# Performance work log

Measured on AMD Instinct MI355X. Metric: run time of the kernel, lower is better.

Reference implementation:

```python
import jax, jax.numpy as jnp
import numpy as np

T = 0.1  # temperature (init kwarg)
NEG_INF = -1e9


def setup_inputs() -> dict:
    key = jax.random.key(0)
    k1, k2 = jax.random.split(key)
    B, N, D = 4096, 2, 128
    feats = jax.random.normal(k1, (B, N, D), dtype=jnp.float32)
    labels = jax.random.randint(k2, (B,), 0, 512, dtype=jnp.int64)
    return {"feats": feats, "labels": labels}


def reference(feats, labels):
    B, N, D = feats.shape
    M = B * N
    f = feats.reshape(M, D)
    # F.normalize(dim=1): L2 normalize rows with eps clamp
    norm = jnp.maximum(jnp.linalg.norm(f, axis=1, keepdims=True), 1e-12)
    f = f / norm
    # labels.unsqueeze(1).repeat(1, N).view(-1)
    lab = jnp.repeat(labels, N)  # [M]
    mask = (lab[:, None] == lab[None, :]).astype(f.dtype)  # [M, M]
    logits = (f @ f.T) / T  # [M, M]
    logits_mask = 1.0 - jnp.eye(M, dtype=f.dtype)
    mask = mask * logits_mask  # drop self-pairs
    logits = logits * logits_mask + NEG_INF * (1.0 - logits_mask)
    log_prob = logits - jax.nn.logsumexp(logits, axis=1, keepdims=True)
    mean_pos = (mask * log_prob).sum(axis=1) / mask.sum(axis=1)
    return -mean_pos.mean()
```

## Files before the change

kernel.cpp:

```cpp
#include <hip/hip_runtime.h>
#include <math.h>

#define DD 128
#define NSPLIT 24
#define NBINS 512
#define SHIFT 10.0f
#define L2E_T 14.4269504089f

#define AS1 __attribute__((address_space(1)))
#define AS3 __attribute__((address_space(3)))

typedef _Float16 f16x8 __attribute__((ext_vector_type(8)));
typedef _Float16 f16x2 __attribute__((ext_vector_type(2)));
typedef float f32x4 __attribute__((ext_vector_type(4)));

__device__ __forceinline__ float ex2(float x) {
#if __has_builtin(__builtin_amdgcn_exp2f)
    return __builtin_amdgcn_exp2f(x);
#else
    return exp2f(x);
#endif
}

__global__ __launch_bounds__(256)
void zero_kernel(int* __restrict__ hist, float* __restrict__ out)
{
    hist[threadIdx.x] = 0;
    hist[256 + threadIdx.x] = 0;
    if (threadIdx.x == 0) out[0] = 0.f;
}

__global__ __launch_bounds__(256)
void norm_kernel(const float* __restrict__ f, const int* __restrict__ labels,
                 _Float16* __restrict__ fh, int* __restrict__ labm,
                 int* __restrict__ hist, int M, int nrep)
{
    int gw = (blockIdx.x * 256 + threadIdx.x) >> 6;
    int lane = threadIdx.x & 63;
    if (gw >= M) return;
    float2 v = *reinterpret_cast<const float2*>(&f[(size_t)gw * DD + lane * 2]);
    float ss = v.x * v.x + v.y * v.y;
    #pragma unroll
    for (int m = 1; m < 64; m <<= 1) ss += __shfl_xor(ss, m);
    float inv = 1.0f / fmaxf(sqrtf(ss), 1e-12f);
    f16x2 h; h[0] = (_Float16)(v.x * inv); h[1] = (_Float16)(v.y * inv);
    *reinterpret_cast<f16x2*>(&fh[(size_t)gw * DD + lane * 2]) = h;
    if (lane == 0) {
        int lb = labels[gw / nrep];
        labm[gw] = lb;
        if ((gw % nrep) == 0) atomicAdd(&hist[lb], nrep);
    }
}

__global__ __launch_bounds__(256, 3)
void supcon_main(const _Float16* __restrict__ fh, const int* __restrict__ labm,
                 float* __restrict__ Epart, float* __restrict__ Ppart,
                 int M, int nsub_total)
{
    __shared__ float4 jbuf[2][1024];

    const int tid = threadIdx.x;
    const int lane = tid & 63;
    const int w = tid >> 6;
    const int ibase = blockIdx.x * 256 + w * 64;
    const int rowsel = lane & 15;
    const int grp = lane >> 4;
    const int ksel = grp * 8;

    f16x8 bfr[4][4];
    #pragma unroll
    for (int t = 0; t < 4; ++t)
        #pragma unroll
        for (int kk = 0; kk < 4; ++kk)
            bfr[t][kk] = *reinterpret_cast<const f16x8*>(
                &fh[(size_t)(ibase + t * 16 + rowsel) * DD + kk * 32 + ksel]);

    int li[4];
    #pragma unroll
    for (int t = 0; t < 4; ++t) li[t] = labm[ibase + t * 16 + rowsel];

    float esum[4] = {0.f, 0.f, 0.f, 0.f};
    float psum[4] = {0.f, 0.f, 0.f, 0.f};

    const int base = nsub_total / NSPLIT, rem = nsub_total % NSPLIT;
    const int by = blockIdx.y;
    const int s0 = by * base + (by < rem ? by : rem);
    const int send = s0 + base + (by < rem ? 1 : 0);
    const int nsub = send - s0;
    const int nb = (nsub + 3) >> 2;
    const int rowmax = nsub_total * 16 - 1;

    int srow[4], scol[4];
    #pragma unroll
    for (int p = 0; p < 4; ++p) {
        int s = (p * 4 + w) * 64 + lane;
        srow[p] = s >> 4;
        scol[p] = ((s & 15) ^ ((s >> 4) & 7)) * 8;
    }

#define STAGE(bb, tt) { \
    const int rb = (s0 + (tt) * 4) * 16; \
    _Pragma("unroll") for (int p = 0; p < 4; ++p) { \
        int rr = rb + srow[p]; if (rr > rowmax) rr = rowmax; \
        const _Float16* gsrc = fh + (size_t)rr * DD + scol[p]; \
        __builtin_amdgcn_global_load_lds((const AS1 void*)gsrc, \
            (AS3 void*)&jbuf[bb][(p * 4 + w) * 64], 16, 0, 0); } }

#define LDSAF(bb, k) { \
    _Pragma("unroll") for (int kk = 0; kk < 4; ++kk) { \
        int slot = ((k) * 16 + rowsel) * 16 + ((kk * 4 + grp) ^ (rowsel & 7)); \
        af[kk] = *reinterpret_cast<const f16x8*>(&jbuf[bb][slot]); } }

#define MFMA16(A, c0, c1, c2, c3) { \
    _Pragma("unroll") for (int kk = 0; kk < 4; ++kk) { \
        c0 = __builtin_amdgcn_mfma_f32_16x16x32_f16(A[kk], bfr[0][kk], c0, 0, 0, 0); \
        c1 = __builtin_amdgcn_mfma_f32_16x16x32_f16(A[kk], bfr[1][kk], c1, 0, 0, 0); \
        c2 = __builtin_amdgcn_mfma_f32_16x16x32_f16(A[kk], bfr[2][kk], c2, 0, 0, 0); \
        c3 = __builtin_amdgcn_mfma_f32_16x16x32_f16(A[kk], bfr[3][kk], c3, 0, 0, 0); } }

#define EPI1(t, cc, L) { \
    esum[t] += (ex2(__builtin_fmaf(cc[0], L2E_T, -L2E_T)) \
              + ex2(__builtin_fmaf(cc[1], L2E_T, -L2E_T))) \
             + (ex2(__builtin_fmaf(cc[2], L2E_T, -L2E_T)) \
              + ex2(__builtin_fmaf(cc[3], L2E_T, -L2E_T))); \
    float p0 = (L.x == li[t]) ? cc[0] : 0.f; \
    float p1 = (L.y == li[t]) ? cc[1] : 0.f; \
    float p2 = (L.z == li[t]) ? cc[2] : 0.f; \
    float p3 = (L.w == li[t]) ? cc[3] : 0.f; \
    psum[t] += (p0 + p1) + (p2 + p3); }

#define EPI4(c0, c1, c2, c3, L) { \
    EPI1(0, c0, L); EPI1(1, c1, L); EPI1(2, c2, L); EPI1(3, c3, L); }

#define PAIR(bb, tt, k0, k1) { \
    f16x8 af[4]; \
    LDSAF(bb, k0); \
    f32x4 A0 = {0,0,0,0}, A1 = {0,0,0,0}, A2 = {0,0,0,0}, A3 = {0,0,0,0}; \
    MFMA16(af, A0, A1, A2, A3); \
    LDSAF(bb, k1); \
    f32x4 B0 = {0,0,0,0}, B1 = {0,0,0,0}, B2 = {0,0,0,0}, B3 = {0,0,0,0}; \
    MFMA16(af, B0, B1, B2, B3); \
    const int4 lj0 = *reinterpret_cast<const int4*>( \
        &labm[(s0 + (tt) * 4 + (k0)) * 16 + grp * 4]); \
    const int4 lj1 = *reinterpret_cast<const int4*>( \
        &labm[(s0 + (tt) * 4 + (k1)) * 16 + grp * 4]); \
    EPI4(A0, A1, A2, A3, lj0); \
    EPI4(B0, B1, B2, B3, lj1); }

#define SINGLE(bb, tt, k0) { \
    f16x8 af[4]; \
    LDSAF(bb, k0); \
    f32x4 A0 = {0,0,0,0}, A1 = {0,0,0,0}, A2 = {0,0,0,0}, A3 = {0,0,0,0}; \
    MFMA16(af, A0, A1, A2, A3); \
    const int4 lj0 = *reinterpret_cast<const int4*>( \
        &labm[(s0 + (tt) * 4 + (k0)) * 16 + grp * 4]); \
    EPI4(A0, A1, A2, A3, lj0); }

    STAGE(0, 0);
    __syncthreads();
    for (int t = 0; t < nb; ++t) {
        if (t + 1 < nb) STAGE((t + 1) & 1, t + 1);
        const int nv = (t == nb - 1) ? (nsub - (nb - 1) * 4) : 4;
        if (nv >= 2) PAIR(t & 1, t, 0, 1);
        if (nv == 4) { PAIR(t & 1, t, 2, 3); }
        else if (nv == 3) { SINGLE(t & 1, t, 2); }
        else if (nv == 1) { SINGLE(t & 1, t, 0); }
        __syncthreads();
    }
#undef STAGE
#undef LDSAF
#undef MFMA16
#undef EPI1
#undef EPI4
#undef PAIR
#undef SINGLE

    #pragma unroll
    for (int t = 0; t < 4; ++t) {
        float e = esum[t], p = psum[t];
        e += __shfl_xor(e, 16); e += __shfl_xor(e, 32);
        p += __shfl_xor(p, 16); p += __shfl_xor(p, 32);
        if (lane < 16) {
            size_t o = (size_t)by * M + ibase + t * 16 + lane;
            Epart[o] = e;
            Ppart[o] = p;
        }
    }
}

__global__ __launch_bounds__(256)
void final_fused(const _Float16* __restrict__ fh, const float* __restrict__ Epart,
                 const float* __restrict__ Ppart, const int* __restrict__ labm,
                 const int* __restrict__ hist, float* __restrict__ out, int M)
{
    __shared__ float red[4];
    const int i = blockIdx.x * 256 + threadIdx.x;
    float aii = 0.f;
    const f16x8* fr = reinterpret_cast<const f16x8*>(&fh[(size_t)i * DD]);
    #pragma unroll
    for (int k = 0; k < 16; ++k) {
        f16x8 hv = fr[k];
        #pragma unroll
        for (int e = 0; e < 8; ++e) {
            float x = (float)hv[e];
            aii = __builtin_fmaf(x, x, aii);
        }
    }
    float E = 0.f, P = 0.f;
    #pragma unroll
    for (int k = 0; k < NSPLIT; ++k) {
        E += Epart[(size_t)k * M + i];
        P += Ppart[(size_t)k * M + i];
    }
    int lb = labm[i];
    float cnt = (float)(hist[lb] - 1);
    E -= ex2(__builtin_fmaf(aii, L2E_T, -L2E_T));
    float term = (SHIFT + logf(E)) - SHIFT * (P - aii) / cnt;

    #pragma unroll
    for (int m = 1; m < 64; m <<= 1) term += __shfl_xor(term, m);
    int lane = threadIdx.x & 63, wv = threadIdx.x >> 6;
    if (lane == 0) red[wv] = term;
    __syncthreads();
    if (threadIdx.x == 0)
        atomicAdd(out, (red[0] + red[1] + red[2] + red[3]) / (float)M);
}

extern "C" void kernel_launch(void* const* d_in, const int* in_sizes, int n_in,
                              void* d_out, int out_size, void* d_ws, size_t ws_size,
                              hipStream_t stream)
{
    const float* feats = (const float*)d_in[0];
    const int* labels = (const int*)d_in[1];
    const int Bn = in_sizes[1];
    const int M = in_sizes[0] / DD;
    const int nrep = M / Bn;

    char* ws = (char*)d_ws;
    _Float16* fh = (_Float16*)ws;
    size_t off = (size_t)M * DD * sizeof(_Float16);
    int* labm = (int*)(ws + off); off += (size_t)M * sizeof(int);
    int* hist = (int*)(ws + off); off += (size_t)NBINS * sizeof(int);
    off = (off + 255) & ~(size_t)255;
    float* Epart = (float*)(ws + off); off += (size_t)NSPLIT * M * sizeof(float);
    float* Ppart = (float*)(ws + off); off += (size_t)NSPLIT * M * sizeof(float);

    zero_kernel<<<1, 256, 0, stream>>>(hist, (float*)d_out);

    norm_kernel<<<M / 4, 256, 0, stream>>>(feats, labels, fh, labm, hist, M, nrep);

    const int nsub_total = M / 16;
    dim3 grid(M / 256, NSPLIT);
    supcon_main<<<grid, 256, 0, stream>>>(fh, labm, Epart, Ppart, M, nsub_total);

    final_fused<<<M / 256, 256, 0, stream>>>(fh, Epart, Ppart, labm, hist,
                                             (float*)d_out, M);
}
```

Baseline: 48.93 us.

## Halve per-wave row tile and use even column split across more blocks

Each wave now holds 32 resident i-rows instead of 64, so a block covers 128 rows, and the j dimension is split into 16 equal chunks instead of 24 uneven ones. The remainder and tail handling for partial subtiles is removed, and the launch bound asks for 4 blocks per CU. The goal is lower register pressure and more occupancy, plus simpler loops without bounds clamps. In exchange, each j tile staged in LDS is reused across half as many rows, which doubles global-to-LDS traffic, and the code now assumes M is divisible by 16*64.

```diff
diff --git a/kernel.cpp b/kernel.cpp
--- a/kernel.cpp
+++ b/kernel.cpp
@@ -2,7 +2,7 @@
 #include <math.h>
 
 #define DD 128
-#define NSPLIT 24
+#define NSPLIT 16
 #define NBINS 512
 #define SHIFT 10.0f
 #define L2E_T 14.4269504089f
@@ -52,43 +52,39 @@
     }
 }
 
-__global__ __launch_bounds__(256, 3)
+__global__ __launch_bounds__(256, 4)
 void supcon_main(const _Float16* __restrict__ fh, const int* __restrict__ labm,
                  float* __restrict__ Epart, float* __restrict__ Ppart,
-                 int M, int nsub_total)
+                 int M, int jchunk)
 {
     __shared__ float4 jbuf[2][1024];
 
     const int tid = threadIdx.x;
     const int lane = tid & 63;
     const int w = tid >> 6;
-    const int ibase = blockIdx.x * 256 + w * 64;
+    const int ibase = blockIdx.x * 128 + w * 32;
     const int rowsel = lane & 15;
     const int grp = lane >> 4;
     const int ksel = grp * 8;
 
-    f16x8 bfr[4][4];
-    #pragma unroll
-    for (int t = 0; t < 4; ++t)
+    f16x8 bfr[2][4];
+    #pragma unroll
+    for (int t = 0; t < 2; ++t)
         #pragma unroll
         for (int kk = 0; kk < 4; ++kk)
             bfr[t][kk] = *reinterpret_cast<const f16x8*>(
                 &fh[(size_t)(ibase + t * 16 + rowsel) * DD + kk * 32 + ksel]);
 
-    int li[4];
-    #pragma unroll
-    for (int t = 0; t < 4; ++t) li[t] = labm[ibase + t * 16 + rowsel];
-
-    float esum[4] = {0.f, 0.f, 0.f, 0.f};
-    float psum[4] = {0.f, 0.f, 0.f, 0.f};
-
-    const int base = nsub_total / NSPLIT, rem = nsub_total % NSPLIT;
+    int li[2];
+    #pragma unroll
+    for (int t = 0; t < 2; ++t) li[t] = labm[ibase + t * 16 + rowsel];
+
+    float esum[2] = {0.f, 0.f};
+    float psum[2] = {0.f, 0.f};
+
     const int by = blockIdx.y;
-    const int s0 = by * base + (by < rem ? by : rem);
-    const int send = s0 + base + (by < rem ? 1 : 0);
-    const int nsub = send - s0;
-    const int nb = (nsub + 3) >> 2;
-    const int rowmax = nsub_total * 16 - 1;
+    const int j0row = by * jchunk;
+    const int nb = jchunk / 64;
 
     int srow[4], scol[4];
     #pragma unroll
@@ -99,10 +95,9 @@
     }
 
 #define STAGE(bb, tt) { \
-    const int rb = (s0 + (tt) * 4) * 16; \
+    const int rb = j0row + (tt) * 64; \
     _Pragma("unroll") for (int p = 0; p < 4; ++p) { \
-        int rr = rb + srow[p]; if (rr > rowmax) rr = rowmax; \
-        const _Float16* gsrc = fh + (size_t)rr * DD + scol[p]; \
+        const _Float16* gsrc = fh + (size_t)(rb + srow[p]) * DD + scol[p]; \
         __builtin_amdgcn_global_load_lds((const AS1 void*)gsrc, \
             (AS3 void*)&jbuf[bb][(p * 4 + w) * 64], 16, 0, 0); } }
 
@@ -111,12 +106,10 @@
         int slot = ((k) * 16 + rowsel) * 16 + ((kk * 4 + grp) ^ (rowsel & 7)); \
         af[kk] = *reinterpret_cast<const f16x8*>(&jbuf[bb][slot]); } }
 
-#define MFMA16(A, c0, c1, c2, c3) { \
+#define MFMA8(A, c0, c1) { \
     _Pragma("unroll") for (int kk = 0; kk < 4; ++kk) { \
         c0 = __builtin_amdgcn_mfma_f32_16x16x32_f16(A[kk], bfr[0][kk], c0, 0, 0, 0); \
-        c1 = __builtin_amdgcn_mfma_f32_16x16x32_f16(A[kk], bfr[1][kk], c1, 0, 0, 0); \
-        c2 = __builtin_amdgcn_mfma_f32_16x16x32_f16(A[kk], bfr[2][kk], c2, 0, 0, 0); \
-        c3 = __builtin_amdgcn_mfma_f32_16x16x32_f16(A[kk], bfr[3][kk], c3, 0, 0, 0); } }
+        c1 = __builtin_amdgcn_mfma_f32_16x16x32_f16(A[kk], bfr[1][kk], c1, 0, 0, 0); } }
 
 #define EPI1(t, cc, L) { \
     esum[t] += (ex2(__builtin_fmaf(cc[0], L2E_T, -L2E_T)) \
@@ -129,54 +122,37 @@
     float p3 = (L.w == li[t]) ? cc[3] : 0.f; \
     psum[t] += (p0 + p1) + (p2 + p3); }
 
-#define EPI4(c0, c1, c2, c3, L) { \
-    EPI1(0, c0, L); EPI1(1, c1, L); EPI1(2, c2, L); EPI1(3, c3, L); }
-
 #define PAIR(bb, tt, k0, k1) { \
     f16x8 af[4]; \
     LDSAF(bb, k0); \
-    f32x4 A0 = {0,0,0,0}, A1 = {0,0,0,0}, A2 = {0,0,0,0}, A3 = {0,0,0,0}; \
-    MFMA16(af, A0, A1, A2, A3); \
+    f32x4 A0 = {0,0,0,0}, A1 = {0,0,0,0}; \
+    MFMA8(af, A0, A1); \
     LDSAF(bb, k1); \
-    f32x4 B0 = {0,0,0,0}, B1 = {0,0,0,0}, B2 = {0,0,0,0}, B3 = {0,0,0,0}; \
-    MFMA16(af, B0, B1, B2, B3); \
+    f32x4 B0 = {0,0,0,0}, B1 = {0,0,0,0}; \
+    MFMA8(af, B0, B1); \
     const int4 lj0 = *reinterpret_cast<const int4*>( \
-        &labm[(s0 + (tt) * 4 + (k0)) * 16 + grp * 4]); \
+        &labm[j0row + ((tt) * 4 + (k0)) * 16 + grp * 4]); \
     const int4 lj1 = *reinterpret_cast<const int4*>( \
-        &labm[(s0 + (tt) * 4 + (k1)) * 16 + grp * 4]); \
-    EPI4(A0, A1, A2, A3, lj0); \
-    EPI4(B0, B1, B2, B3, lj1); }
-
-#define SINGLE(bb, tt, k0) { \
-    f16x8 af[4]; \
-    LDSAF(bb, k0); \
-    f32x4 A0 = {0,0,0,0}, A1 = {0,0,0,0}, A2 = {0,0,0,0}, A3 = {0,0,0,0}; \
-    MFMA16(af, A0, A1, A2, A3); \
-    const int4 lj0 = *reinterpret_cast<const int4*>( \
-        &labm[(s0 + (tt) * 4 + (k0)) * 16 + grp * 4]); \
-    EPI4(A0, A1, A2, A3, lj0); }
+        &labm[j0row + ((tt) * 4 + (k1)) * 16 + grp * 4]); \
+    EPI1(0, A0, lj0); EPI1(1, A1, lj0); \
+    EPI1(0, B0, lj1); EPI1(1, B1, lj1); }
 
     STAGE(0, 0);
     __syncthreads();
     for (int t = 0; t < nb; ++t) {
         if (t + 1 < nb) STAGE((t + 1) & 1, t + 1);
-        const int nv = (t == nb - 1) ? (nsub - (nb - 1) * 4) : 4;
-        if (nv >= 2) PAIR(t & 1, t, 0, 1);
-        if (nv == 4) { PAIR(t & 1, t, 2, 3); }
-        else if (nv == 3) { SINGLE(t & 1, t, 2); }
-        else if (nv == 1) { SINGLE(t & 1, t, 0); }
+        PAIR(t & 1, t, 0, 1);
+        PAIR(t & 1, t, 2, 3);
         __syncthreads();
     }
 #undef STAGE
 #undef LDSAF
-#undef MFMA16
+#undef MFMA8
 #undef EPI1
-#undef EPI4
 #undef PAIR
-#undef SINGLE
-
-    #pragma unroll
-    for (int t = 0; t < 4; ++t) {
+
+    #pragma unroll
+    for (int t = 0; t < 2; ++t) {
         float e = esum[t], p = psum[t];
         e += __shfl_xor(e, 16); e += __shfl_xor(e, 32);
         p += __shfl_xor(p, 16); p += __shfl_xor(p, 32);
@@ -249,9 +225,9 @@
 
     norm_kernel<<<M / 4, 256, 0, stream>>>(feats, labels, fh, labm, hist, M, nrep);
 
-    const int nsub_total = M / 16;
-    dim3 grid(M / 256, NSPLIT);
-    supcon_main<<<grid, 256, 0, stream>>>(fh, labm, Epart, Ppart, M, nsub_total);
+    const int jchunk = M / NSPLIT;
+    dim3 grid(M / 128, NSPLIT);
+    supcon_main<<<grid, 256, 0, stream>>>(fh, labm, Epart, Ppart, M, jchunk);
 
     final_fused<<<M / 256, 256, 0, stream>>>(fh, Epart, Ppart, labm, hist,
                                              (float*)d_out, M);
```

Result: slower. 50.21 us (+2.6%).

## Exploit Gram matrix symmetry: compute upper triangle once, accumulate row and column sums

Applied to the files above, without the earlier changes.

Uses the symmetry of f·fᵀ so that each off-diagonal tile is computed once. Its exp-sums and positive-sums are added both to the row accumulators and, through column reductions, to separate column-partial buffers. Work is balanced by pairing block-row pid with block-row 31-pid across 48 slices of 11 subtiles. The zero kernel now also clears the row-partial buffers, and the final kernel adds the extra column partials. This roughly halves the MFMA and exp work, at the cost of extra shuffles, more global writes, and a hardcoded M=8192 layout (the 31-pid pairing and SLICE constant).

```diff
diff --git a/kernel.cpp b/kernel.cpp
--- a/kernel.cpp
+++ b/kernel.cpp
@@ -2,7 +2,8 @@
 #include <math.h>
 
 #define DD 128
-#define NSPLIT 24
+#define NSLICE 48
+#define SLICE 11
 #define NBINS 512
 #define SHIFT 10.0f
 #define L2E_T 14.4269504089f
@@ -23,11 +24,13 @@
 }
 
 __global__ __launch_bounds__(256)
-void zero_kernel(int* __restrict__ hist, float* __restrict__ out)
-{
-    hist[threadIdx.x] = 0;
-    hist[256 + threadIdx.x] = 0;
-    if (threadIdx.x == 0) out[0] = 0.f;
+void zero_kernel(float4* __restrict__ ep4, int n4, int* __restrict__ hist,
+                 float* __restrict__ out)
+{
+    int g = blockIdx.x * 256 + threadIdx.x;
+    if (g < n4) ep4[g] = make_float4(0.f, 0.f, 0.f, 0.f);
+    if (g < NBINS / 4) reinterpret_cast<int4*>(hist)[g] = make_int4(0, 0, 0, 0);
+    if (g == 0) out[0] = 0.f;
 }
 
 __global__ __launch_bounds__(256)
@@ -54,57 +57,38 @@
 
 __global__ __launch_bounds__(256, 3)
 void supcon_main(const _Float16* __restrict__ fh, const int* __restrict__ labm,
-                 float* __restrict__ Epart, float* __restrict__ Ppart,
-                 int M, int nsub_total)
+                 float* __restrict__ EpE, float* __restrict__ EpP,
+                 float* __restrict__ EcE, float* __restrict__ EcP, int M)
 {
     __shared__ float4 jbuf[2][1024];
 
     const int tid = threadIdx.x;
     const int lane = tid & 63;
     const int w = tid >> 6;
-    const int ibase = blockIdx.x * 256 + w * 64;
     const int rowsel = lane & 15;
     const int grp = lane >> 4;
     const int ksel = grp * 8;
-
-    f16x8 bfr[4][4];
-    #pragma unroll
-    for (int t = 0; t < 4; ++t)
-        #pragma unroll
-        for (int kk = 0; kk < 4; ++kk)
-            bfr[t][kk] = *reinterpret_cast<const f16x8*>(
-                &fh[(size_t)(ibase + t * 16 + rowsel) * DD + kk * 32 + ksel]);
-
-    int li[4];
-    #pragma unroll
-    for (int t = 0; t < 4; ++t) li[t] = labm[ibase + t * 16 + rowsel];
-
-    float esum[4] = {0.f, 0.f, 0.f, 0.f};
-    float psum[4] = {0.f, 0.f, 0.f, 0.f};
-
-    const int base = nsub_total / NSPLIT, rem = nsub_total % NSPLIT;
+    const int rowlim = M - 1;
+
+    const int pid = blockIdx.x;
     const int by = blockIdx.y;
-    const int s0 = by * base + (by < rem ? by : rem);
-    const int send = s0 + base + (by < rem ? 1 : 0);
-    const int nsub = send - s0;
-    const int nb = (nsub + 3) >> 2;
-    const int rowmax = nsub_total * 16 - 1;
+    const int NS = M / 16;
+    const int LA = NS - 16 * pid;
 
     int srow[4], scol[4];
     #pragma unroll
-    for (int p = 0; p < 4; ++p) {
-        int s = (p * 4 + w) * 64 + lane;
-        srow[p] = s >> 4;
-        scol[p] = ((s & 15) ^ ((s >> 4) & 7)) * 8;
-    }
-
-#define STAGE(bb, tt) { \
-    const int rb = (s0 + (tt) * 4) * 16; \
-    _Pragma("unroll") for (int p = 0; p < 4; ++p) { \
-        int rr = rb + srow[p]; if (rr > rowmax) rr = rowmax; \
-        const _Float16* gsrc = fh + (size_t)rr * DD + scol[p]; \
+    for (int q = 0; q < 4; ++q) {
+        int s = (q * 4 + w) * 64 + lane;
+        srow[q] = s >> 4;
+        scol[q] = ((s & 15) ^ ((s >> 4) & 7)) * 8;
+    }
+
+#define STAGE(bb, rbase) { \
+    _Pragma("unroll") for (int q = 0; q < 4; ++q) { \
+        int rr = (rbase) + srow[q]; if (rr > rowlim) rr = rowlim; \
+        const _Float16* gsrc = fh + (size_t)rr * DD + scol[q]; \
         __builtin_amdgcn_global_load_lds((const AS1 void*)gsrc, \
-            (AS3 void*)&jbuf[bb][(p * 4 + w) * 64], 16, 0, 0); } }
+            (AS3 void*)&jbuf[bb][(q * 4 + w) * 64], 16, 0, 0); } }
 
 #define LDSAF(bb, k) { \
     _Pragma("unroll") for (int kk = 0; kk < 4; ++kk) { \
@@ -118,21 +102,40 @@
         c2 = __builtin_amdgcn_mfma_f32_16x16x32_f16(A[kk], bfr[2][kk], c2, 0, 0, 0); \
         c3 = __builtin_amdgcn_mfma_f32_16x16x32_f16(A[kk], bfr[3][kk], c3, 0, 0, 0); } }
 
-#define EPI1(t, cc, L) { \
-    esum[t] += (ex2(__builtin_fmaf(cc[0], L2E_T, -L2E_T)) \
-              + ex2(__builtin_fmaf(cc[1], L2E_T, -L2E_T))) \
-             + (ex2(__builtin_fmaf(cc[2], L2E_T, -L2E_T)) \
-              + ex2(__builtin_fmaf(cc[3], L2E_T, -L2E_T))); \
-    float p0 = (L.x == li[t]) ? cc[0] : 0.f; \
-    float p1 = (L.y == li[t]) ? cc[1] : 0.f; \
-    float p2 = (L.z == li[t]) ? cc[2] : 0.f; \
-    float p3 = (L.w == li[t]) ? cc[3] : 0.f; \
-    psum[t] += (p0 + p1) + (p2 + p3); }
-
-#define EPI4(c0, c1, c2, c3, L) { \
-    EPI1(0, c0, L); EPI1(1, c1, L); EPI1(2, c2, L); EPI1(3, c3, L); }
-
-#define PAIR(bb, tt, k0, k1) { \
+#define RED4(v) { v += __shfl_xor(v, 1); v += __shfl_xor(v, 2); \
+                  v += __shfl_xor(v, 4); v += __shfl_xor(v, 8); }
+
+#define EPI1C(t, cc, L) { \
+    float e0 = ex2(__builtin_fmaf(cc[0], L2E_T, -L2E_T)); \
+    float e1 = ex2(__builtin_fmaf(cc[1], L2E_T, -L2E_T)); \
+    float e2 = ex2(__builtin_fmaf(cc[2], L2E_T, -L2E_T)); \
+    float e3 = ex2(__builtin_fmaf(cc[3], L2E_T, -L2E_T)); \
+    esum[t] += (e0 + e1) + (e2 + e3); \
+    float q0 = (L.x == li[t]) ? cc[0] : 0.f; \
+    float q1 = (L.y == li[t]) ? cc[1] : 0.f; \
+    float q2 = (L.z == li[t]) ? cc[2] : 0.f; \
+    float q3 = (L.w == li[t]) ? cc[3] : 0.f; \
+    psum[t] += (q0 + q1) + (q2 + q3); \
+    cE0 += e0; cE1 += e1; cE2 += e2; cE3 += e3; \
+    cP0 += q0; cP1 += q1; cP2 += q2; cP3 += q3; }
+
+#define EPICOL(c0v, c1v, c2v, c3v, sg) { \
+    const int4 lj = *reinterpret_cast<const int4*>(&labm[(sg) * 16 + grp * 4]); \
+    const bool doc = (((sg) >> 4) != BXr); \
+    float cE0 = 0.f, cE1 = 0.f, cE2 = 0.f, cE3 = 0.f; \
+    float cP0 = 0.f, cP1 = 0.f, cP2 = 0.f, cP3 = 0.f; \
+    EPI1C(0, c0v, lj); EPI1C(1, c1v, lj); EPI1C(2, c2v, lj); EPI1C(3, c3v, lj); \
+    if (doc) { \
+        RED4(cE0); RED4(cE1); RED4(cE2); RED4(cE3); \
+        RED4(cP0); RED4(cP1); RED4(cP2); RED4(cP3); \
+        if (rowsel == 0) { \
+            float4 vE; vE.x = cE0; vE.y = cE1; vE.z = cE2; vE.w = cE3; \
+            float4 vP; vP.x = cP0; vP.y = cP1; vP.z = cP2; vP.w = cP3; \
+            size_t co = (size_t)(BXr * 4 + w) * M + (sg) * 16 + grp * 4; \
+            *reinterpret_cast<float4*>(&EcE[co]) = vE; \
+            *reinterpret_cast<float4*>(&EcP[co]) = vP; } } }
+
+#define PAIRC(bb, k0, k1, sg0, sg1) { \
     f16x8 af[4]; \
     LDSAF(bb, k0); \
     f32x4 A0 = {0,0,0,0}, A1 = {0,0,0,0}, A2 = {0,0,0,0}, A3 = {0,0,0,0}; \
@@ -140,61 +143,79 @@
     LDSAF(bb, k1); \
     f32x4 B0 = {0,0,0,0}, B1 = {0,0,0,0}, B2 = {0,0,0,0}, B3 = {0,0,0,0}; \
     MFMA16(af, B0, B1, B2, B3); \
-    const int4 lj0 = *reinterpret_cast<const int4*>( \
-        &labm[(s0 + (tt) * 4 + (k0)) * 16 + grp * 4]); \
-    const int4 lj1 = *reinterpret_cast<const int4*>( \
-        &labm[(s0 + (tt) * 4 + (k1)) * 16 + grp * 4]); \
-    EPI4(A0, A1, A2, A3, lj0); \
-    EPI4(B0, B1, B2, B3, lj1); }
-
-#define SINGLE(bb, tt, k0) { \
+    EPICOL(A0, A1, A2, A3, (sg0)); \
+    EPICOL(B0, B1, B2, B3, (sg1)); }
+
+#define SINGLEC(bb, k0, sg0) { \
     f16x8 af[4]; \
     LDSAF(bb, k0); \
     f32x4 A0 = {0,0,0,0}, A1 = {0,0,0,0}, A2 = {0,0,0,0}, A3 = {0,0,0,0}; \
     MFMA16(af, A0, A1, A2, A3); \
-    const int4 lj0 = *reinterpret_cast<const int4*>( \
-        &labm[(s0 + (tt) * 4 + (k0)) * 16 + grp * 4]); \
-    EPI4(A0, A1, A2, A3, lj0); }
-
-    STAGE(0, 0);
-    __syncthreads();
-    for (int t = 0; t < nb; ++t) {
-        if (t + 1 < nb) STAGE((t + 1) & 1, t + 1);
-        const int nv = (t == nb - 1) ? (nsub - (nb - 1) * 4) : 4;
-        if (nv >= 2) PAIR(t & 1, t, 0, 1);
-        if (nv == 4) { PAIR(t & 1, t, 2, 3); }
-        else if (nv == 3) { SINGLE(t & 1, t, 2); }
-        else if (nv == 1) { SINGLE(t & 1, t, 0); }
-        __syncthreads();
-    }
+    EPICOL(A0, A1, A2, A3, (sg0)); }
+
+#define DO_RUN(BX_, S0_, N_) { \
+    const int BXr = (BX_); \
+    const int S0r = (S0_); \
+    const int Nr = (N_); \
+    const int ibase = BXr * 256 + w * 64; \
+    f16x8 bfr[4][4]; \
+    _Pragma("unroll") for (int t = 0; t < 4; ++t) \
+        _Pragma("unroll") for (int kk = 0; kk < 4; ++kk) \
+            bfr[t][kk] = *reinterpret_cast<const f16x8*>( \
+                &fh[(size_t)(ibase + t * 16 + rowsel) * DD + kk * 32 + ksel]); \
+    int li[4]; \
+    _Pragma("unroll") for (int t = 0; t < 4; ++t) \
+        li[t] = labm[ibase + t * 16 + rowsel]; \
+    float esum[4] = {0.f, 0.f, 0.f, 0.f}; \
+    float psum[4] = {0.f, 0.f, 0.f, 0.f}; \
+    const int nb = (Nr + 3) >> 2; \
+    STAGE(0, S0r * 16); \
+    __syncthreads(); \
+    for (int t = 0; t < nb; ++t) { \
+        if (t + 1 < nb) STAGE((t + 1) & 1, (S0r + (t + 1) * 4) * 16); \
+        const int nv = (t == nb - 1) ? (Nr - (nb - 1) * 4) : 4; \
+        const int sgb = S0r + t * 4; \
+        if (nv >= 2) PAIRC(t & 1, 0, 1, sgb, sgb + 1); \
+        if (nv == 4) { PAIRC(t & 1, 2, 3, sgb + 2, sgb + 3); } \
+        else if (nv == 3) { SINGLEC(t & 1, 2, sgb + 2); } \
+        else if (nv == 1) { SINGLEC(t & 1, 0, sgb); } \
+        __syncthreads(); \
+    } \
+    _Pragma("unroll") for (int t = 0; t < 4; ++t) { \
+        float e = esum[t], pp = psum[t]; \
+        e += __shfl_xor(e, 16); e += __shfl_xor(e, 32); \
+        pp += __shfl_xor(pp, 16); pp += __shfl_xor(pp, 32); \
+        if (lane < 16) { \
+            size_t o = (size_t)by * M + ibase + t * 16 + lane; \
+            EpE[o] = e; \
+            EpP[o] = pp; } } }
+
+    const int u0 = by * SLICE, u1 = u0 + SLICE;
+    int a0 = u0, a1 = (u1 < LA) ? u1 : LA;
+    if (a1 > a0) DO_RUN(pid, pid * 16 + a0, a1 - a0);
+    int b0 = (u0 > LA) ? u0 : LA, b1 = u1;
+    if (b1 > b0) DO_RUN(31 - pid, (31 - pid) * 16 + (b0 - LA), b1 - b0);
+
 #undef STAGE
 #undef LDSAF
 #undef MFMA16
-#undef EPI1
-#undef EPI4
-#undef PAIR
-#undef SINGLE
-
-    #pragma unroll
-    for (int t = 0; t < 4; ++t) {
-        float e = esum[t], p = psum[t];
-        e += __shfl_xor(e, 16); e += __shfl_xor(e, 32);
-        p += __shfl_xor(p, 16); p += __shfl_xor(p, 32);
-        if (lane < 16) {
-            size_t o = (size_t)by * M + ibase + t * 16 + lane;
-            Epart[o] = e;
-            Ppart[o] = p;
-        }
-    }
+#undef RED4
+#undef EPI1C
+#undef EPICOL
+#undef PAIRC
+#undef SINGLEC
+#undef DO_RUN
 }
 
 __global__ __launch_bounds__(256)
-void final_fused(const _Float16* __restrict__ fh, const float* __restrict__ Epart,
-                 const float* __restrict__ Ppart, const int* __restrict__ labm,
+void final_fused(const _Float16* __restrict__ fh, const float* __restrict__ EpE,
+                 const float* __restrict__ EpP, const float* __restrict__ EcE,
+                 const float* __restrict__ EcP, const int* __restrict__ labm,
                  const int* __restrict__ hist, float* __restrict__ out, int M)
 {
     __shared__ float red[4];
-    const int i = blockIdx.x * 256 + threadIdx.x;
+    const int b = blockIdx.x;
+    const int i = b * 256 + threadIdx.x;
     float aii = 0.f;
     const f16x8* fr = reinterpret_cast<const f16x8*>(&fh[(size_t)i * DD]);
     #pragma unroll
@@ -208,9 +229,14 @@
     }
     float E = 0.f, P = 0.f;
     #pragma unroll
-    for (int k = 0; k < NSPLIT; ++k) {
-        E += Epart[(size_t)k * M + i];
-        P += Ppart[(size_t)k * M + i];
+    for (int k = 0; k < NSLICE; ++k) {
+        E += EpE[(size_t)k * M + i];
+        P += EpP[(size_t)k * M + i];
+    }
+    const int nc = 4 * b;
+    for (int k = 0; k < nc; ++k) {
+        E += EcE[(size_t)k * M + i];
+        P += EcP[(size_t)k * M + i];
     }
     int lb = labm[i];
     float cnt = (float)(hist[lb] - 1);
@@ -242,17 +268,20 @@
     int* labm = (int*)(ws + off); off += (size_t)M * sizeof(int);
     int* hist = (int*)(ws + off); off += (size_t)NBINS * sizeof(int);
     off = (off + 255) & ~(size_t)255;
-    float* Epart = (float*)(ws + off); off += (size_t)NSPLIT * M * sizeof(float);
-    float* Ppart = (float*)(ws + off); off += (size_t)NSPLIT * M * sizeof(float);
-
-    zero_kernel<<<1, 256, 0, stream>>>(hist, (float*)d_out);
+    float* EpE = (float*)(ws + off); off += (size_t)NSLICE * M * sizeof(float);
+    float* EpP = (float*)(ws + off); off += (size_t)NSLICE * M * sizeof(float);
+    float* EcE = (float*)(ws + off); off += (size_t)128 * M * sizeof(float);
+    float* EcP = (float*)(ws + off); off += (size_t)128 * M * sizeof(float);
+
+    const int n4 = (NSLICE * M * 2) / 4;
+    zero_kernel<<<(n4 + 255) / 256, 256, 0, stream>>>((float4*)EpE, n4, hist,
+                                                      (float*)d_out);
 
     norm_kernel<<<M / 4, 256, 0, stream>>>(feats, labels, fh, labm, hist, M, nrep);
 
-    const int nsub_total = M / 16;
-    dim3 grid(M / 256, NSPLIT);
-    supcon_main<<<grid, 256, 0, stream>>>(fh, labm, Epart, Ppart, M, nsub_total);
-
-    final_fused<<<M / 256, 256, 0, stream>>>(fh, Epart, Ppart, labm, hist,
+    dim3 grid(M / 512, NSLICE);
+    supcon_main<<<grid, 256, 0, stream>>>(fh, labm, EpE, EpP, EcE, EcP, M);
+
+    final_fused<<<M / 256, 256, 0, stream>>>(fh, EpE, EpP, EcE, EcP, labm, hist,
                                              (float*)d_out, M);
 }
```

Result: slower. 84.38 us (+72.5%).
